# Kernel optimization log

Measured on AMD Instinct MI355X. Metric: run time of the kernel, lower is better.

## Reference

```python
import jax, jax.numpy as jnp
import numpy as np

H = 128  # hidden size
I = 6    # input size after concat

def setup_inputs() -> dict:
    key = jax.random.key(0)
    ks = jax.random.split(key, 12)
    B, T = 2048, 168
    s_inp = jax.random.normal(ks[0], (B, T, 5), dtype=jnp.float32)
    flow_x = jax.random.normal(ks[1], (B, T, 1), dtype=jnp.float32)
    sc = 1.0 / np.sqrt(H)
    # PyTorch LSTM params: gate order i, f, g, o
    W_ih = jax.random.uniform(ks[2], (4 * H, I), jnp.float32, -sc, sc)
    W_hh = jax.random.uniform(ks[3], (4 * H, H), jnp.float32, -sc, sc)
    b_ih = jax.random.uniform(ks[4], (4 * H,), jnp.float32, -sc, sc)
    b_hh = jax.random.uniform(ks[5], (4 * H,), jnp.float32, -sc, sc)
    sc1 = 1.0 / np.sqrt(128)
    W1 = jax.random.uniform(ks[6], (64, 128), jnp.float32, -sc1, sc1)
    b1 = jax.random.uniform(ks[7], (64,), jnp.float32, -sc1, sc1)
    a1 = jnp.array(0.25, dtype=jnp.float32)  # PReLU weight
    sc2 = 1.0 / np.sqrt(64)
    W2 = jax.random.uniform(ks[8], (1, 64), jnp.float32, -sc2, sc2)
    b2 = jax.random.uniform(ks[9], (1,), jnp.float32, -sc2, sc2)
    a2 = jnp.array(0.25, dtype=jnp.float32)
    return {"s_inp": s_inp, "flow_x": flow_x, "W_ih": W_ih, "W_hh": W_hh,
            "b_ih": b_ih, "b_hh": b_hh, "W1": W1, "b1": b1, "a1": a1,
            "W2": W2, "b2": b2, "a2": a2}

def _prelu(x, a):
    return jnp.where(x >= 0, x, a * x)

def _lstm_last(x, W_ih, W_hh, b_ih, b_hh):
    # x: [B, T, I] -> last hidden state h_T: [B, H]
    B = x.shape[0]
    # precompute input contribution for all timesteps: [T, B, 4H]
    x_gates = jnp.einsum('bti,gi->tbg', x, W_ih) + (b_ih + b_hh)

    def step(carry, xg):
        h, c = carry
        gates = xg + h @ W_hh.T  # [B, 4H]
        i, f, g, o = jnp.split(gates, 4, axis=-1)
        i = jax.nn.sigmoid(i)
        f = jax.nn.sigmoid(f)
        g = jnp.tanh(g)
        o = jax.nn.sigmoid(o)
        c = f * c + i * g
        h = o * jnp.tanh(c)
        return (h, c), None

    h0 = jnp.zeros((B, H), dtype=x.dtype)
    c0 = jnp.zeros((B, H), dtype=x.dtype)
    (h, c), _ = jax.lax.scan(step, (h0, c0), x_gates)
    return h

def reference(s_inp, flow_x, W_ih, W_hh, b_ih, b_hh, W1, b1, a1, W2, b2, a2):
    x = jnp.concatenate([s_inp, flow_x], axis=2)  # [B, T, 6]
    h_last = _lstm_last(x, W_ih, W_hh, b_ih, b_hh)  # [B, 128]
    y = _prelu(h_last @ W1.T + b1, a1)              # [B, 64]
    y = _prelu(y @ W2.T + b2, a2)                   # [B, 1]
    return y
```

## Files before the change

### kernel.cpp

```cpp
#include <hip/hip_runtime.h>


typedef __attribute__((ext_vector_type(8))) short short8;
typedef __attribute__((ext_vector_type(4))) float f32x4;

#define BT 512
#define TS 168
#define HID 128
#define ROWSTR 192
#define NKK 5
#define NNT 4

__device__ __forceinline__ ushort bf_hi(float v) {
    return (ushort)(__float_as_uint(v) >> 16);
}
__device__ __forceinline__ ushort bf_lo(float v) {
    unsigned h = __float_as_uint(v) & 0xFFFF0000u;
    float l = v - __uint_as_float(h);
    return (ushort)(__float_as_uint(l) >> 16);
}
__device__ __forceinline__ float sigm_f(float x) {
    return __fdividef(1.f, 1.f + __expf(-x));
}
__device__ __forceinline__ float tanh_f(float x) {
    return 1.f - __fdividef(2.f, __expf(2.f * x) + 1.f);
}

__global__ __launch_bounds__(BT, 2) void lstm_mfma3_kernel(
    const float* __restrict__ s_inp,
    const float* __restrict__ flow_x,
    const float* __restrict__ W_ih,
    const float* __restrict__ W_hh,
    const float* __restrict__ b_ih,
    const float* __restrict__ b_hh,
    const float* __restrict__ W1,
    const float* __restrict__ b1,
    const float* __restrict__ a1p,
    const float* __restrict__ W2,
    const float* __restrict__ b2,
    const float* __restrict__ a2p,
    float* __restrict__ out)
{
    __shared__ float xs[8][TS][6];
    __shared__ __align__(16) ushort hA[16 * ROWSTR];
    __shared__ float y1s[8][64];

    const int t = threadIdx.x;
    const int w = t >> 6;
    const int l = t & 63;
    const int l15 = l & 15;
    const int l4 = l >> 4;
    const int row_base = blockIdx.x * 8;

    short8 Bh[NKK][NNT], Bl[NKK][NNT];
    #pragma unroll
    for (int nt = 0; nt < NNT; ++nt) {
        const int gc = nt * HID + w * 16 + l15;
        const float bias = b_ih[gc] + b_hh[gc];
        #pragma unroll
        for (int kk = 0; kk < NKK; ++kk) {
            #pragma unroll
            for (int j = 0; j < 8; ++j) {
                int k = kk * 32 + l4 * 8 + j;
                float v;
                if (k < HID)           v = W_hh[gc * HID + k];
                else if (k < HID + 6)  v = W_ih[gc * 6 + (k - HID)];
                else if (k == HID + 6) v = bias;
                else                   v = 0.f;
                Bh[kk][nt][j] = (short)bf_hi(v);
                Bl[kk][nt][j] = (short)bf_lo(v);
            }
        }
    }

    for (int idx = t; idx < 8 * TS * 5; idx += BT) {
        int r = idx / (TS * 5), rem = idx % (TS * 5);
        xs[r][rem / 5][rem % 5] = s_inp[(size_t)row_base * (TS * 5) + idx];
    }
    for (int idx = t; idx < 8 * TS; idx += BT) {
        xs[idx / TS][idx % TS][5] = flow_x[(size_t)row_base * TS + idx];
    }
    for (int idx = t; idx < 16 * ROWSTR / 2; idx += BT)
        ((unsigned*)hA)[idx] = 0u;
    __syncthreads();

    if (t < 8) {
        int byte = (2 * 134) ^ ((t & 7) << 4);
        hA[t * ROWSTR + (byte >> 1)] = 0x3F80;
    }
    const bool xhi = (t < 48);
    const bool xlo = (t >= 64 && t < 112);
    const int xu = xhi ? t : (t - 64);
    const int xr = (xu < 48) ? (xu / 6) : 0;
    const int xi = (xu < 48) ? (xu % 6) : 0;
    const int xw_idx = ((xhi ? xr : xr + 8) * ROWSTR) +
                       (((2 * (HID + xi)) ^ ((xr & 7) << 4)) >> 1);
    if (xhi | xlo) {
        float v = xs[xr][0][xi];
        hA[xw_idx] = xhi ? bf_hi(v) : bf_lo(v);
    }

    const int a_base = l15 * ROWSTR;
    const int a_swz = (l15 & 7) << 4;
    const int ch = w * 16 + l15;
    const bool lowhalf = (l < 32);
    const int rbase = (l4 & 1) * 4 + (lowhalf ? 0 : 2);
    const int row0 = rbase, row1 = rbase + 1;
    const int cb0 = (2 * ch) ^ ((row0 & 7) << 4);
    const int cb1 = (2 * ch) ^ ((row1 & 7) << 4);
    const int hw00 = row0 * ROWSTR + (cb0 >> 1);
    const int hw01 = (row0 + 8) * ROWSTR + (cb0 >> 1);
    const int hw10 = row1 * ROWSTR + (cb1 >> 1);
    const int hw11 = (row1 + 8) * ROWSTR + (cb1 >> 1);

    float c0 = 0.f, c1 = 0.f, h0f = 0.f, h1f = 0.f;

    for (int s = 0; s < TS; ++s) {
        __syncthreads();

        f32x4 D1[NNT], D2[NNT];
        #pragma unroll
        for (int nt = 0; nt < NNT; ++nt) {
            D1[nt] = (f32x4){0.f, 0.f, 0.f, 0.f};
            D2[nt] = (f32x4){0.f, 0.f, 0.f, 0.f};
        }

        #pragma unroll
        for (int kk = 0; kk < NKK; ++kk) {
            int off = ((kk * 64 + l4 * 16) ^ a_swz) >> 1;
            short8 a = *(const short8*)(hA + a_base + off);
            #pragma unroll
            for (int nt = 0; nt < NNT; ++nt)
                D1[nt] = __builtin_amdgcn_mfma_f32_16x16x32_bf16(a, Bh[kk][nt], D1[nt], 0, 0, 0);
            #pragma unroll
            for (int nt = 0; nt < NNT; ++nt)
                D2[nt] = __builtin_amdgcn_mfma_f32_16x16x32_bf16(a, Bl[kk][nt], D2[nt], 0, 0, 0);
        }

        float gate[NNT][2];
        #pragma unroll
        for (int nt = 0; nt < NNT; ++nt) {
            f32x4 s4;
            #pragma unroll
            for (int r = 0; r < 4; ++r) s4[r] = D1[nt][r] + D2[nt][r];
            #pragma unroll
            for (int r = 0; r < 4; ++r) s4[r] += __shfl_xor(s4[r], 32, 64);
            gate[nt][0] = lowhalf ? s4[0] : s4[2];
            gate[nt][1] = lowhalf ? s4[1] : s4[3];
        }

        {
            float ia = sigm_f(gate[0][0]);
            float fa = sigm_f(gate[1][0]);
            float ga = tanh_f(gate[2][0]);
            float oa = sigm_f(gate[3][0]);
            c0 = fa * c0 + ia * ga;
            h0f = oa * tanh_f(c0);
        }
        {
            float ia = sigm_f(gate[0][1]);
            float fa = sigm_f(gate[1][1]);
            float ga = tanh_f(gate[2][1]);
            float oa = sigm_f(gate[3][1]);
            c1 = fa * c1 + ia * ga;
            h1f = oa * tanh_f(c1);
        }

        hA[hw00] = bf_hi(h0f);
        hA[hw01] = bf_lo(h0f);
        hA[hw10] = bf_hi(h1f);
        hA[hw11] = bf_lo(h1f);

        if ((xhi | xlo) && s + 1 < TS) {
            float v = xs[xr][s + 1][xi];
            hA[xw_idx] = xhi ? bf_hi(v) : bf_lo(v);
        }
    }
    __syncthreads();

    float* hfin = (float*)xs;
    hfin[row0 * HID + ch] = h0f;
    hfin[row1 * HID + ch] = h1f;
    __syncthreads();

    {
        int r = t >> 6, j = t & 63;
        const float4* wrow = (const float4*)(W1 + j * HID);
        const float4* hr = (const float4*)(hfin + r * HID);
        float acc = b1[j];
        #pragma unroll
        for (int q = 0; q < HID / 4; ++q) {
            float4 a = hr[q], b = wrow[q];
            acc += a.x * b.x + a.y * b.y + a.z * b.z + a.w * b.w;
        }
        float av = a1p[0];
        y1s[r][j] = (acc >= 0.f) ? acc : av * acc;
    }
    __syncthreads();

    if (t < 8) {
        const float4* w2 = (const float4*)W2;
        const float4* yr = (const float4*)&y1s[t][0];
        float acc = 0.f;
        #pragma unroll
        for (int q = 0; q < 64 / 4; ++q) {
            float4 a = yr[q], b = w2[q];
            acc += a.x * b.x + a.y * b.y + a.z * b.z + a.w * b.w;
        }
        acc += b2[0];
        float av = a2p[0];
        out[row_base + t] = (acc >= 0.f) ? acc : av * acc;
    }
}

extern "C" void kernel_launch(void* const* d_in, const int* in_sizes, int n_in,
                              void* d_out, int out_size, void* d_ws, size_t ws_size,
                              hipStream_t stream) {
    const float* s_inp  = (const float*)d_in[0];
    const float* flow_x = (const float*)d_in[1];
    const float* W_ih   = (const float*)d_in[2];
    const float* W_hh   = (const float*)d_in[3];
    const float* b_ih   = (const float*)d_in[4];
    const float* b_hh   = (const float*)d_in[5];
    const float* b1_    = (const float*)d_in[7];
    const float* W1     = (const float*)d_in[6];
    const float* a1     = (const float*)d_in[8];
    const float* W2     = (const float*)d_in[9];
    const float* b2     = (const float*)d_in[10];
    const float* a2     = (const float*)d_in[11];
    float* out = (float*)d_out;

    dim3 grid(2048 / 8);
    dim3 block(BT);
    lstm_mfma3_kernel<<<grid, block, 0, stream>>>(
        s_inp, flow_x, W_ih, W_hh, b_ih, b_hh, W1, b1_, a1, W2, b2, a2, out);
}
```

Measured before the change: 253.1 us.

## Fold bf16 hi/lo split into the K dimension and drop the cross-half shuffle

```diff
diff --git a/kernel.cpp b/kernel.cpp
--- a/kernel.cpp
+++ b/kernel.cpp
@@ -7,8 +7,7 @@
 #define BT 512
 #define TS 168
 #define HID 128
-#define ROWSTR 192
-#define NKK 5
+#define AROW 320
 #define NNT 4
 
 __device__ __forceinline__ ushort bf_hi(float v) {
@@ -26,7 +25,7 @@
     return 1.f - __fdividef(2.f, __expf(2.f * x) + 1.f);
 }
 
-__global__ __launch_bounds__(BT, 2) void lstm_mfma3_kernel(
+__global__ __launch_bounds__(BT, 2) void lstm_mfma6_kernel(
     const float* __restrict__ s_inp,
     const float* __restrict__ flow_x,
     const float* __restrict__ W_ih,
@@ -42,7 +41,7 @@
     float* __restrict__ out)
 {
     __shared__ float xs[8][TS][6];
-    __shared__ __align__(16) ushort hA[16 * ROWSTR];
+    __shared__ __align__(16) ushort hA[8 * AROW];
     __shared__ float y1s[8][64];
 
     const int t = threadIdx.x;
@@ -52,24 +51,28 @@
     const int l4 = l >> 4;
     const int row_base = blockIdx.x * 8;
 
-    short8 Bh[NKK][NNT], Bl[NKK][NNT];
+    short8 P1s[5][NNT], P2s[5][NNT];
     #pragma unroll
     for (int nt = 0; nt < NNT; ++nt) {
         const int gc = nt * HID + w * 16 + l15;
         const float bias = b_ih[gc] + b_hh[gc];
         #pragma unroll
-        for (int kk = 0; kk < NKK; ++kk) {
+        for (int q = 0; q < 4; ++q) {
             #pragma unroll
             for (int j = 0; j < 8; ++j) {
-                int k = kk * 32 + l4 * 8 + j;
-                float v;
-                if (k < HID)           v = W_hh[gc * HID + k];
-                else if (k < HID + 6)  v = W_ih[gc * 6 + (k - HID)];
-                else if (k == HID + 6) v = bias;
-                else                   v = 0.f;
-                Bh[kk][nt][j] = (short)bf_hi(v);
-                Bl[kk][nt][j] = (short)bf_lo(v);
+                float v = W_hh[gc * HID + q * 32 + l4 * 8 + j];
+                P1s[q][nt][j] = (short)bf_hi(v);
+                P2s[q][nt][j] = (short)bf_lo(v);
             }
+        }
+        #pragma unroll
+        for (int j = 0; j < 8; ++j) {
+            int u = l4 * 8 + j;
+            float v = (u < 6)  ? W_ih[gc * 6 + u]
+                    : (u < 12) ? W_ih[gc * 6 + (u - 6)]
+                    : (u == 12) ? bias : 0.f;
+            P1s[4][nt][j] = (short)bf_hi(v);
+            P2s[4][nt][j] = (short)bf_lo(v);
         }
     }
 
@@ -80,96 +83,90 @@
     for (int idx = t; idx < 8 * TS; idx += BT) {
         xs[idx / TS][idx % TS][5] = flow_x[(size_t)row_base * TS + idx];
     }
-    for (int idx = t; idx < 16 * ROWSTR / 2; idx += BT)
+    for (int idx = t; idx < 8 * AROW / 2; idx += BT)
         ((unsigned*)hA)[idx] = 0u;
     __syncthreads();
 
     if (t < 8) {
-        int byte = (2 * 134) ^ ((t & 7) << 4);
-        hA[t * ROWSTR + (byte >> 1)] = 0x3F80;
+        int byte = (2 * 268) ^ ((t & 7) << 4);
+        hA[t * AROW + (byte >> 1)] = 0x3F80;
     }
     const bool xhi = (t < 48);
     const bool xlo = (t >= 64 && t < 112);
     const int xu = xhi ? t : (t - 64);
     const int xr = (xu < 48) ? (xu / 6) : 0;
     const int xi = (xu < 48) ? (xu % 6) : 0;
-    const int xw_idx = ((xhi ? xr : xr + 8) * ROWSTR) +
-                       (((2 * (HID + xi)) ^ ((xr & 7) << 4)) >> 1);
+    const int xslot = xhi ? (256 + xi) : (262 + xi);
+    const int xw_idx = xr * AROW + ((((2 * xslot) ^ ((xr & 7) << 4))) >> 1);
     if (xhi | xlo) {
         float v = xs[xr][0][xi];
         hA[xw_idx] = xhi ? bf_hi(v) : bf_lo(v);
     }
 
-    const int a_base = l15 * ROWSTR;
-    const int a_swz = (l15 & 7) << 4;
+    const int arow = l15 & 7;
+    const int a_base = arow * AROW;
+    const int a_swz = arow << 4;
     const int ch = w * 16 + l15;
     const bool lowhalf = (l < 32);
     const int rbase = (l4 & 1) * 4 + (lowhalf ? 0 : 2);
     const int row0 = rbase, row1 = rbase + 1;
-    const int cb0 = (2 * ch) ^ ((row0 & 7) << 4);
-    const int cb1 = (2 * ch) ^ ((row1 & 7) << 4);
-    const int hw00 = row0 * ROWSTR + (cb0 >> 1);
-    const int hw01 = (row0 + 8) * ROWSTR + (cb0 >> 1);
-    const int hw10 = row1 * ROWSTR + (cb1 >> 1);
-    const int hw11 = (row1 + 8) * ROWSTR + (cb1 >> 1);
+    const int hw0 = row0 * AROW + ((((2 * ch) ^ (row0 << 4))) >> 1);
+    const int hw1 = row1 * AROW + ((((2 * ch) ^ (row1 << 4))) >> 1);
 
     float c0 = 0.f, c1 = 0.f, h0f = 0.f, h1f = 0.f;
 
     for (int s = 0; s < TS; ++s) {
         __syncthreads();
 
-        f32x4 D1[NNT], D2[NNT];
-        #pragma unroll
-        for (int nt = 0; nt < NNT; ++nt) {
-            D1[nt] = (f32x4){0.f, 0.f, 0.f, 0.f};
-            D2[nt] = (f32x4){0.f, 0.f, 0.f, 0.f};
-        }
-
-        #pragma unroll
-        for (int kk = 0; kk < NKK; ++kk) {
+        f32x4 acc[NNT];
+        #pragma unroll
+        for (int nt = 0; nt < NNT; ++nt) acc[nt] = (f32x4){0.f, 0.f, 0.f, 0.f};
+
+        #pragma unroll
+        for (int kk = 0; kk < 9; ++kk) {
+            const int q = (kk < 4) ? kk : ((kk < 8) ? kk - 4 : 4);
             int off = ((kk * 64 + l4 * 16) ^ a_swz) >> 1;
             short8 a = *(const short8*)(hA + a_base + off);
             #pragma unroll
             for (int nt = 0; nt < NNT; ++nt)
-                D1[nt] = __builtin_amdgcn_mfma_f32_16x16x32_bf16(a, Bh[kk][nt], D1[nt], 0, 0, 0);
-            #pragma unroll
-            for (int nt = 0; nt < NNT; ++nt)
-                D2[nt] = __builtin_amdgcn_mfma_f32_16x16x32_bf16(a, Bl[kk][nt], D2[nt], 0, 0, 0);
-        }
-
-        float gate[NNT][2];
-        #pragma unroll
-        for (int nt = 0; nt < NNT; ++nt) {
-            f32x4 s4;
-            #pragma unroll
-            for (int r = 0; r < 4; ++r) s4[r] = D1[nt][r] + D2[nt][r];
-            #pragma unroll
-            for (int r = 0; r < 4; ++r) s4[r] += __shfl_xor(s4[r], 32, 64);
-            gate[nt][0] = lowhalf ? s4[0] : s4[2];
-            gate[nt][1] = lowhalf ? s4[1] : s4[3];
-        }
+                acc[nt] = __builtin_amdgcn_mfma_f32_16x16x32_bf16(a, P1s[q][nt], acc[nt], 0, 0, 0);
+            if (kk < 4 || kk == 8) {
+                #pragma unroll
+                for (int nt = 0; nt < NNT; ++nt)
+                    acc[nt] = __builtin_amdgcn_mfma_f32_16x16x32_bf16(a, P2s[q][nt], acc[nt], 0, 0, 0);
+            }
+        }
+
+        float gi0 = lowhalf ? acc[0][0] : acc[0][2];
+        float gf0 = lowhalf ? acc[1][0] : acc[1][2];
+        float gg0 = lowhalf ? acc[2][0] : acc[2][2];
+        float go0 = lowhalf ? acc[3][0] : acc[3][2];
+        float gi1 = lowhalf ? acc[0][1] : acc[0][3];
+        float gf1 = lowhalf ? acc[1][1] : acc[1][3];
+        float gg1 = lowhalf ? acc[2][1] : acc[2][3];
+        float go1 = lowhalf ? acc[3][1] : acc[3][3];
 
         {
-            float ia = sigm_f(gate[0][0]);
-            float fa = sigm_f(gate[1][0]);
-            float ga = tanh_f(gate[2][0]);
-            float oa = sigm_f(gate[3][0]);
+            float ia = sigm_f(gi0);
+            float fa = sigm_f(gf0);
+            float ga = tanh_f(gg0);
+            float oa = sigm_f(go0);
             c0 = fa * c0 + ia * ga;
             h0f = oa * tanh_f(c0);
         }
         {
-            float ia = sigm_f(gate[0][1]);
-            float fa = sigm_f(gate[1][1]);
-            float ga = tanh_f(gate[2][1]);
-            float oa = sigm_f(gate[3][1]);
+            float ia = sigm_f(gi1);
+            float fa = sigm_f(gf1);
+            float ga = tanh_f(gg1);
+            float oa = sigm_f(go1);
             c1 = fa * c1 + ia * ga;
             h1f = oa * tanh_f(c1);
         }
 
-        hA[hw00] = bf_hi(h0f);
-        hA[hw01] = bf_lo(h0f);
-        hA[hw10] = bf_hi(h1f);
-        hA[hw11] = bf_lo(h1f);
+        hA[hw0] = bf_hi(h0f);
+        hA[hw0 + 128] = bf_lo(h0f);
+        hA[hw1] = bf_hi(h1f);
+        hA[hw1 + 128] = bf_lo(h1f);
 
         if ((xhi | xlo) && s + 1 < TS) {
             float v = xs[xr][s + 1][xi];
@@ -222,8 +219,8 @@
     const float* W_hh   = (const float*)d_in[3];
     const float* b_ih   = (const float*)d_in[4];
     const float* b_hh   = (const float*)d_in[5];
-    const float* b1_    = (const float*)d_in[7];
     const float* W1     = (const float*)d_in[6];
+    const float* b1     = (const float*)d_in[7];
     const float* a1     = (const float*)d_in[8];
     const float* W2     = (const float*)d_in[9];
     const float* b2     = (const float*)d_in[10];
@@ -232,6 +229,6 @@
 
     dim3 grid(2048 / 8);
     dim3 block(BT);
-    lstm_mfma3_kernel<<<grid, block, 0, stream>>>(
-        s_inp, flow_x, W_ih, W_hh, b_ih, b_hh, W1, b1_, a1, W2, b2, a2, out);
-}
+    lstm_mfma6_kernel<<<grid, block, 0, stream>>>(
+        s_inp, flow_x, W_ih, W_hh, b_ih, b_hh, W1, b1, a1, W2, b2, a2, out);
+}
```

New measurement: 261.1 us. +3.2%, slower.
